# Kernel tuning notes

Hardware: AMD Instinct MI355X
Metric: run time of the kernel (lower is better)

The kernel has to match this reference:

```python
import jax, jax.numpy as jnp
import numpy as np

B, T, C = 2, 2048, 2048
N_HEAD, KV_HEADS = 16, 4
HEAD_DIM = C // N_HEAD  # 128
EPS = 1e-6


def setup_inputs() -> dict:
    key = jax.random.key(0)
    ks = jax.random.split(key, 3)
    x = jax.random.normal(ks[0], (B, T, C), dtype=jnp.float32)
    qkv_out = (N_HEAD + 2 * KV_HEADS) * HEAD_DIM  # 3072
    w_qkv = jax.random.normal(ks[1], (qkv_out, C), dtype=jnp.float32) * 0.02
    w_proj = jax.random.normal(ks[2], (C, C), dtype=jnp.float32) * 0.02
    q_norm_w = jnp.ones((HEAD_DIM,), dtype=jnp.float32)
    k_norm_w = jnp.ones((HEAD_DIM,), dtype=jnp.float32)
    # RoPE frequencies: theta = 10000^{-2i/d}, angles = pos * theta
    inv_freq = 1.0 / (10000.0 ** (np.arange(0, HEAD_DIM, 2, dtype=np.float32) / HEAD_DIM))
    angles = np.arange(T, dtype=np.float32)[:, None] * inv_freq[None, :]  # [T, 64]
    freqs_cos = jnp.asarray(np.cos(angles), dtype=jnp.float32)
    freqs_sin = jnp.asarray(np.sin(angles), dtype=jnp.float32)
    return {"x": x, "w_qkv": w_qkv, "w_proj": w_proj,
            "q_norm_w": q_norm_w, "k_norm_w": k_norm_w,
            "freqs_cos": freqs_cos, "freqs_sin": freqs_sin}


def _rope(t, cos, sin):
    # t: [B, H, T, D]; interpret last dim as D/2 complex pairs (a, b)
    a = t[..., 0::2]
    b = t[..., 1::2]
    oa = a * cos - b * sin
    ob = a * sin + b * cos
    return jnp.stack([oa, ob], axis=-1).reshape(t.shape)


def _rmsnorm(t, w, eps=EPS):
    rms = jnp.sqrt(jnp.mean(t * t, axis=-1, keepdims=True) + eps)
    return w * (t / rms)


def reference(x, w_qkv, w_proj, q_norm_w, k_norm_w, freqs_cos, freqs_sin):
    b, t, c = x.shape
    hd = HEAD_DIM
    qkv = x @ w_qkv.T  # [B, T, 3072]
    q_size = N_HEAD * hd
    kv_size = KV_HEADS * hd
    q = qkv[..., :q_size].reshape(b, t, N_HEAD, hd).transpose(0, 2, 1, 3)
    k = qkv[..., q_size:q_size + kv_size].reshape(b, t, KV_HEADS, hd).transpose(0, 2, 1, 3)
    v = qkv[..., q_size + kv_size:].reshape(b, t, KV_HEADS, hd).transpose(0, 2, 1, 3)
    # repeat_interleave KV heads to match query heads (GQA)
    rep = N_HEAD // KV_HEADS
    k = jnp.repeat(k, rep, axis=1)
    v = jnp.repeat(v, rep, axis=1)
    # RoPE (applied after repeat, matching the torch code order)
    cos = freqs_cos[:t][None, None, :, :]
    sin = freqs_sin[:t][None, None, :, :]
    q = _rope(q, cos, sin)
    k = _rope(k, cos, sin)
    # QK RMSNorm per head_dim
    q = _rmsnorm(q, q_norm_w)
    k = _rmsnorm(k, k_norm_w)
    # causal SDPA
    scores = jnp.einsum('bhqd,bhkd->bhqk', q, k) / jnp.sqrt(jnp.float32(hd))
    causal = jnp.tril(jnp.ones((t, t), dtype=bool))
    scores = jnp.where(causal[None, None], scores, jnp.finfo(scores.dtype).min)
    att = jax.nn.softmax(scores, axis=-1)
    y = jnp.einsum('bhqk,bhkd->bhqd', att, v)
    y = y.transpose(0, 2, 1, 3).reshape(b, t, c)
    return y @ w_proj.T
```

## Files before the change

### kernel.cpp

```cpp
#include <hip/hip_runtime.h>
#include <hip/hip_bf16.h>

#define B_    2
#define T_    2048
#define C_    2048
#define NH_   16
#define KVH_  4
#define HD_   128
#define QKV_  3072
#define M_    4096

typedef float  floatx4 __attribute__((ext_vector_type(4)));
typedef __bf16 bf16x8  __attribute__((ext_vector_type(8)));
typedef __bf16 bf16x4  __attribute__((ext_vector_type(4)));
typedef __bf16 bf16x2  __attribute__((ext_vector_type(2)));

typedef const __attribute__((address_space(1))) void* gas_t;
typedef __attribute__((address_space(3))) void*       las_t;
__device__ __forceinline__ void gl_lds16(const void* g, void* l) {
  __builtin_amdgcn_global_load_lds((gas_t)g, (las_t)l, 16, 0, 0);
}

__global__ __launch_bounds__(256) void cvt_bf16(const float* __restrict__ src,
                                                __bf16* __restrict__ dst, int n4) {
  int i = blockIdx.x * blockDim.x + threadIdx.x;
  if (i < n4) {
    float4 f = ((const float4*)src)[i];
    bf16x4 o = { (__bf16)f.x, (__bf16)f.y, (__bf16)f.z, (__bf16)f.w };
    ((bf16x4*)dst)[i] = o;
  }
}

__global__ __launch_bounds__(256) void gemm_bt(const __bf16* __restrict__ A,
                                               const __bf16* __restrict__ Bm,
                                               float* __restrict__ Cc,
                                               int N, int K) {
  __shared__ __align__(16) __bf16 As[128 * 32];
  __shared__ __align__(16) __bf16 Bs[128 * 32];
  const int tid  = threadIdx.x;
  const int wid  = tid >> 6, lane = tid & 63, quad = lane >> 4, r16 = lane & 15;
  const int bm   = blockIdx.y * 128, bn = blockIdx.x * 128;
  const int wm   = (wid >> 1) * 64, wn = (wid & 1) * 64;
  const int srow = wid * 16 + (lane >> 2);
  const int scol = (lane & 3) * 8;
  const __bf16* aptr = A  + (size_t)(bm + srow) * K + scol;
  const __bf16* bptr = Bm + (size_t)(bn + srow) * K + scol;
  __bf16* ldsA0 = &As[wid * 512];
  __bf16* ldsA1 = &As[2048 + wid * 512];
  __bf16* ldsB0 = &Bs[wid * 512];
  __bf16* ldsB1 = &Bs[2048 + wid * 512];
  const size_t rowskip = (size_t)64 * K;

  floatx4 acc[4][4];
  #pragma unroll
  for (int i = 0; i < 4; i++)
    #pragma unroll
    for (int j = 0; j < 4; j++) acc[i][j] = (floatx4){0.f, 0.f, 0.f, 0.f};

  for (int k0 = 0; k0 < K; k0 += 32) {
    gl_lds16(aptr + k0,           ldsA0);
    gl_lds16(aptr + rowskip + k0, ldsA1);
    gl_lds16(bptr + k0,           ldsB0);
    gl_lds16(bptr + rowskip + k0, ldsB1);
    __syncthreads();

    bf16x8 af[4], bfr[4];
    #pragma unroll
    for (int i = 0; i < 4; i++) af[i]  = *(const bf16x8*)&As[(wm + i * 16 + r16) * 32 + quad * 8];
    #pragma unroll
    for (int j = 0; j < 4; j++) bfr[j] = *(const bf16x8*)&Bs[(wn + j * 16 + r16) * 32 + quad * 8];

    #pragma unroll
    for (int i = 0; i < 4; i++)
      #pragma unroll
      for (int j = 0; j < 4; j++)
        acc[i][j] = __builtin_amdgcn_mfma_f32_16x16x32_bf16(af[i], bfr[j], acc[i][j], 0, 0, 0);
    __syncthreads();
  }

  #pragma unroll
  for (int i = 0; i < 4; i++) {
    #pragma unroll
    for (int reg = 0; reg < 4; reg++) {
      int row = bm + wm + i * 16 + quad * 4 + reg;
      float* crow = Cc + (size_t)row * N + bn + wn;
      #pragma unroll
      for (int j = 0; j < 4; j++) crow[j * 16 + r16] = acc[i][j][reg];
    }
  }
}

__global__ __launch_bounds__(256) void rope_norm(const float* __restrict__ qkv,
                                                 const float* __restrict__ qw,
                                                 const float* __restrict__ kw,
                                                 const float* __restrict__ fc,
                                                 const float* __restrict__ fs,
                                                 __bf16* __restrict__ qn,
                                                 __bf16* __restrict__ kn) {
  const int tid  = threadIdx.x;
  const int wid  = tid >> 6, lane = tid & 63;
  const int row  = blockIdx.x * 4 + wid;
  const int b    = row >> 11, t = row & (T_ - 1);
  const float cs = fc[t * 64 + lane], sn = fs[t * 64 + lane];
  const float* base = qkv + (size_t)row * QKV_;

  #pragma unroll 2
  for (int h = 0; h < NH_; h++) {
    float2 ab = *(const float2*)(base + h * HD_ + 2 * lane);
    float oa = ab.x * cs - ab.y * sn;
    float ob = ab.x * sn + ab.y * cs;
    float ss = oa * oa + ob * ob;
    #pragma unroll
    for (int off = 32; off; off >>= 1) ss += __shfl_xor(ss, off);
    float rinv = rsqrtf(ss * (1.0f / HD_) + 1e-6f);
    bf16x2 o = { (__bf16)(oa * rinv * qw[2 * lane]), (__bf16)(ob * rinv * qw[2 * lane + 1]) };
    *(bf16x2*)&qn[(size_t)((b * NH_ + h) * T_ + t) * HD_ + 2 * lane] = o;
  }
  #pragma unroll 2
  for (int h = 0; h < KVH_; h++) {
    float2 ab = *(const float2*)(base + C_ + h * HD_ + 2 * lane);
    float oa = ab.x * cs - ab.y * sn;
    float ob = ab.x * sn + ab.y * cs;
    float ss = oa * oa + ob * ob;
    #pragma unroll
    for (int off = 32; off; off >>= 1) ss += __shfl_xor(ss, off);
    float rinv = rsqrtf(ss * (1.0f / HD_) + 1e-6f);
    bf16x2 o = { (__bf16)(oa * rinv * kw[2 * lane]), (__bf16)(ob * rinv * kw[2 * lane + 1]) };
    *(bf16x2*)&kn[(size_t)((b * KVH_ + h) * T_ + t) * HD_ + 2 * lane] = o;
  }
}

__global__ __launch_bounds__(256) void vtrans(const float* __restrict__ qkv,
                                              __bf16* __restrict__ vT) {
  __shared__ __bf16 L[64 * 68];
  const int tid = threadIdx.x;
  const int t0 = blockIdx.x * 64;
  const int d0 = blockIdx.y * 64;
  const int z  = blockIdx.z;
  const int b  = z >> 2, hk = z & 3;
  const int srcc = C_ + KVH_ * HD_ + hk * HD_ + d0;
  const int rr = tid >> 4, c4 = (tid & 15) * 4;
  #pragma unroll
  for (int i = 0; i < 4; i++) {
    int t = rr + i * 16;
    float4 f = *(const float4*)&qkv[(size_t)(b * T_ + t0 + t) * QKV_ + srcc + c4];
    bf16x4 o = { (__bf16)f.x, (__bf16)f.y, (__bf16)f.z, (__bf16)f.w };
    *(bf16x4*)&L[t * 68 + c4] = o;
  }
  __syncthreads();
  const int dr = tid >> 3, tc8 = (tid & 7) * 8;
  #pragma unroll
  for (int i = 0; i < 2; i++) {
    int d = dr + i * 32;
    bf16x8 ov;
    #pragma unroll
    for (int j = 0; j < 8; j++) ov[j] = L[(tc8 + j) * 68 + d];
    *(bf16x8*)&vT[(size_t)(z * HD_ + d0 + d) * T_ + t0 + tc8] = ov;
  }
}

__device__ __forceinline__ void kv_prefetch(const __bf16* kbase, const __bf16* vbase,
                                            int kt0, int wid, int lane,
                                            bf16x8 kreg[4], bf16x8 vreg[4]) {
  const int r4 = lane >> 2, c8 = (lane & 3) * 8;
  const __bf16* kg = kbase + (size_t)(kt0 + wid * 16 + r4) * HD_ + c8;
  #pragma unroll
  for (int cb = 0; cb < 4; cb++) kreg[cb] = *(const bf16x8*)(kg + cb * 32);
  #pragma unroll
  for (int s = 0; s < 2; s++) {
    const __bf16* vg = vbase + (size_t)((wid * 2 + s) * 16 + r4) * T_ + kt0 + c8;
    #pragma unroll
    for (int cb = 0; cb < 2; cb++) vreg[s * 2 + cb] = *(const bf16x8*)(vg + cb * 32);
  }
}

__device__ __forceinline__ void kv_commit(__bf16* Ks, __bf16* Vs, int wid, int lane,
                                          const bf16x8 kreg[4], const bf16x8 vreg[4]) {
  #pragma unroll
  for (int cb = 0; cb < 4; cb++)
    *(bf16x8*)(Ks + wid * 2048 + cb * 512 + lane * 8) = kreg[cb];
  #pragma unroll
  for (int s = 0; s < 2; s++)
    #pragma unroll
    for (int cb = 0; cb < 2; cb++)
      *(bf16x8*)(Vs + (wid * 2 + s) * 1024 + cb * 512 + lane * 8) = vreg[s * 2 + cb];
}

__global__ __launch_bounds__(256) void flash(const __bf16* __restrict__ q,
                                             const __bf16* __restrict__ k,
                                             const __bf16* __restrict__ vT,
                                             __bf16* __restrict__ y) {
  __shared__ __align__(16) __bf16 Ks[64 * 128];
  __shared__ __align__(16) __bf16 Vs[128 * 64];
  __shared__ __align__(16) __bf16 Ps[4][16 * 72];
  const int tid = threadIdx.x;
  const int wid = tid >> 6, lane = tid & 63, quad = lane >> 4, r16 = lane & 15;
  const int h = blockIdx.y, b = blockIdx.z;
  const int hk = h >> 2;
  const __bf16* kbase = k  + (size_t)(b * KVH_ + hk) * T_ * HD_;
  const __bf16* vbase = vT + (size_t)(b * KVH_ + hk) * HD_ * T_;
  __bf16* Pw = Ps[wid];
  const float sc = 0.08838834764831845f;
  const float NEG = -__builtin_inff();
  bf16x8 ones;
  #pragma unroll
  for (int i = 0; i < 8; i++) ones[i] = (__bf16)1.0f;

  #pragma unroll 1
  for (int pass = 0; pass < 2; ++pass) {
    const int qt = pass ? blockIdx.x : (31 - blockIdx.x);
    const int nt = qt + 1;
    const int r0 = qt * 64 + wid * 16;

    const __bf16* qrow = q + ((size_t)(b * NH_ + h) * T_ + r0 + r16) * HD_;
    bf16x8 qf[4];
    #pragma unroll
    for (int kb = 0; kb < 4; kb++) qf[kb] = *(const bf16x8*)&qrow[kb * 32 + quad * 8];

    floatx4 o[8], ol = (floatx4){0.f, 0.f, 0.f, 0.f};
    #pragma unroll
    for (int j = 0; j < 8; j++) o[j] = (floatx4){0.f, 0.f, 0.f, 0.f};
    float m_r[4] = {NEG, NEG, NEG, NEG};

    bf16x8 kreg[4], vreg[4];
    kv_prefetch(kbase, vbase, 0, wid, lane, kreg, vreg);

    #pragma unroll 1
    for (int it = 0; it < nt; ++it) {
      __syncthreads();
      kv_commit(Ks, Vs, wid, lane, kreg, vreg);
      __syncthreads();
      if (it + 1 < nt) kv_prefetch(kbase, vbase, (it + 1) * 64, wid, lane, kreg, vreg);

      const int kt0 = it * 64;
      floatx4 s[4];
      #pragma unroll
      for (int cb = 0; cb < 4; cb++) s[cb] = (floatx4){0.f, 0.f, 0.f, 0.f};
      #pragma unroll
      for (int kb = 0; kb < 4; kb++)
        #pragma unroll
        for (int cb = 0; cb < 4; cb++) {
          bf16x8 kf = *(const bf16x8*)&Ks[(cb * 4 + kb) * 512 + r16 * 32 + quad * 8];
          s[cb] = __builtin_amdgcn_mfma_f32_16x16x32_bf16(qf[kb], kf, s[cb], 0, 0, 0);
        }

      const bool last = (it == nt - 1);
      float alpha[4];
      #pragma unroll
      for (int reg = 0; reg < 4; reg++) {
        const int rowq = r0 + quad * 4 + reg;
        float v0 = s[0][reg] * sc, v1 = s[1][reg] * sc, v2 = s[2][reg] * sc, v3 = s[3][reg] * sc;
        if (last) {
          if (kt0 +      r16 > rowq) v0 = NEG;
          if (kt0 + 16 + r16 > rowq) v1 = NEG;
          if (kt0 + 32 + r16 > rowq) v2 = NEG;
          if (kt0 + 48 + r16 > rowq) v3 = NEG;
        }
        float mx = fmaxf(fmaxf(v0, v1), fmaxf(v2, v3));
        #pragma unroll
        for (int off = 8; off; off >>= 1) mx = fmaxf(mx, __shfl_xor(mx, off));
        float mnew = fmaxf(m_r[reg], mx);
        alpha[reg] = __expf(m_r[reg] - mnew);
        m_r[reg] = mnew;
        Pw[(quad * 4 + reg) * 72 +      r16] = (__bf16)__expf(v0 - mnew);
        Pw[(quad * 4 + reg) * 72 + 16 + r16] = (__bf16)__expf(v1 - mnew);
        Pw[(quad * 4 + reg) * 72 + 32 + r16] = (__bf16)__expf(v2 - mnew);
        Pw[(quad * 4 + reg) * 72 + 48 + r16] = (__bf16)__expf(v3 - mnew);
      }
      #pragma unroll
      for (int reg = 0; reg < 4; reg++) {
        ol[reg] *= alpha[reg];
        #pragma unroll
        for (int j = 0; j < 8; j++) o[j][reg] *= alpha[reg];
      }
      __asm__ volatile("" ::: "memory");
      bf16x8 pf0 = *(const bf16x8*)&Pw[r16 * 72 + quad * 8];
      bf16x8 pf1 = *(const bf16x8*)&Pw[r16 * 72 + 32 + quad * 8];
      ol = __builtin_amdgcn_mfma_f32_16x16x32_bf16(pf0, ones, ol, 0, 0, 0);
      ol = __builtin_amdgcn_mfma_f32_16x16x32_bf16(pf1, ones, ol, 0, 0, 0);
      #pragma unroll
      for (int j = 0; j < 8; j++) {
        bf16x8 vf0 = *(const bf16x8*)&Vs[(j * 2 + 0) * 512 + r16 * 32 + quad * 8];
        bf16x8 vf1 = *(const bf16x8*)&Vs[(j * 2 + 1) * 512 + r16 * 32 + quad * 8];
        o[j] = __builtin_amdgcn_mfma_f32_16x16x32_bf16(pf0, vf0, o[j], 0, 0, 0);
        o[j] = __builtin_amdgcn_mfma_f32_16x16x32_bf16(pf1, vf1, o[j], 0, 0, 0);
      }
    }

    #pragma unroll
    for (int reg = 0; reg < 4; reg++) {
      int trow = r0 + quad * 4 + reg;
      float inv = 1.0f / ol[reg];
      __bf16* yr = y + ((size_t)(b * T_) + trow) * C_ + h * HD_;
      #pragma unroll
      for (int j = 0; j < 8; j++) yr[j * 16 + r16] = (__bf16)(o[j][reg] * inv);
    }
  }
}

extern "C" void kernel_launch(void* const* d_in, const int* in_sizes, int n_in,
                              void* d_out, int out_size, void* d_ws, size_t ws_size,
                              hipStream_t stream) {
  const float* x     = (const float*)d_in[0];
  const float* wqkv  = (const float*)d_in[1];
  const float* wproj = (const float*)d_in[2];
  const float* qw    = (const float*)d_in[3];
  const float* kw    = (const float*)d_in[4];
  const float* fc    = (const float*)d_in[5];
  const float* fs    = (const float*)d_in[6];
  float* out = (float*)d_out;

  char* w = (char*)d_ws;
  __bf16* xb     = (__bf16*)w; w += (size_t)M_ * C_ * 2;
  __bf16* wqkvb  = (__bf16*)w; w += (size_t)QKV_ * C_ * 2;
  __bf16* wprojb = (__bf16*)w; w += (size_t)C_ * C_ * 2;
  float*  qkv    = (float*)w;  w += (size_t)M_ * QKV_ * 4;
  __bf16* qn     = (__bf16*)w; w += (size_t)B_ * NH_ * T_ * HD_ * 2;
  __bf16* kn     = (__bf16*)w; w += (size_t)B_ * KVH_ * T_ * HD_ * 2;
  __bf16* vT     = (__bf16*)w; w += (size_t)B_ * KVH_ * T_ * HD_ * 2;
  __bf16* ybf    = (__bf16*)w; w += (size_t)M_ * C_ * 2;

  cvt_bf16<<<M_ * C_ / 4 / 256, 256, 0, stream>>>(x, xb, M_ * C_ / 4);
  cvt_bf16<<<QKV_ * C_ / 4 / 256, 256, 0, stream>>>(wqkv, wqkvb, QKV_ * C_ / 4);
  cvt_bf16<<<C_ * C_ / 4 / 256, 256, 0, stream>>>(wproj, wprojb, C_ * C_ / 4);

  gemm_bt<<<dim3(QKV_ / 128, M_ / 128), 256, 0, stream>>>(xb, wqkvb, qkv, QKV_, C_);
  rope_norm<<<M_ / 4, 256, 0, stream>>>(qkv, qw, kw, fc, fs, qn, kn);
  vtrans<<<dim3(T_ / 64, HD_ / 64, B_ * KVH_), 256, 0, stream>>>(qkv, vT);
  flash<<<dim3(16, NH_, B_), 256, 0, stream>>>(qn, kn, vT, ybf);
  gemm_bt<<<dim3(C_ / 128, M_ / 128), 256, 0, stream>>>(ybf, wprojb, out, C_, C_);
}
```

Measured before the change: 362.1 us.

## Merge conversions, store QKV in bf16, widen GEMM K-step, restructure flash blocks

The three fp32-to-bf16 conversions become a single launch. The QKV GEMM now writes bf16 instead of fp32, which halves the intermediate traffic read by rope_norm and vtrans. The GEMM loads two 32-wide K slices per barrier pair, halving the number of syncs. The flash kernel moves to 512-thread blocks covering 128 query rows over a flattened 256-block grid, and each warp skips KV tiles that lie entirely above its causal diagonal. Rounding QKV to bf16 before RoPE and the norm adds some precision loss.

Result: faster. 327.4 us (-9.6%).

```diff
diff --git a/kernel.cpp b/kernel.cpp
--- a/kernel.cpp
+++ b/kernel.cpp
@@ -21,22 +21,29 @@
   __builtin_amdgcn_global_load_lds((gas_t)g, (las_t)l, 16, 0, 0);
 }
 
-__global__ __launch_bounds__(256) void cvt_bf16(const float* __restrict__ src,
-                                                __bf16* __restrict__ dst, int n4) {
+__global__ __launch_bounds__(256) void cvt3(const float* __restrict__ s0, __bf16* __restrict__ d0, int n0,
+                                            const float* __restrict__ s1, __bf16* __restrict__ d1, int n1,
+                                            const float* __restrict__ s2, __bf16* __restrict__ d2, int n2) {
   int i = blockIdx.x * blockDim.x + threadIdx.x;
-  if (i < n4) {
-    float4 f = ((const float4*)src)[i];
-    bf16x4 o = { (__bf16)f.x, (__bf16)f.y, (__bf16)f.z, (__bf16)f.w };
-    ((bf16x4*)dst)[i] = o;
-  }
-}
-
+  const float* s; __bf16* d;
+  if (i < n0) { s = s0; d = d0; }
+  else {
+    i -= n0;
+    if (i < n1) { s = s1; d = d1; }
+    else { i -= n1; if (i >= n2) return; s = s2; d = d2; }
+  }
+  float4 f = ((const float4*)s)[i];
+  bf16x4 o = { (__bf16)f.x, (__bf16)f.y, (__bf16)f.z, (__bf16)f.w };
+  ((bf16x4*)d)[i] = o;
+}
+
+template <typename OutT>
 __global__ __launch_bounds__(256) void gemm_bt(const __bf16* __restrict__ A,
                                                const __bf16* __restrict__ Bm,
-                                               float* __restrict__ Cc,
+                                               OutT* __restrict__ Cc,
                                                int N, int K) {
-  __shared__ __align__(16) __bf16 As[128 * 32];
-  __shared__ __align__(16) __bf16 Bs[128 * 32];
+  __shared__ __align__(16) __bf16 As[2][128 * 32];
+  __shared__ __align__(16) __bf16 Bs[2][128 * 32];
   const int tid  = threadIdx.x;
   const int wid  = tid >> 6, lane = tid & 63, quad = lane >> 4, r16 = lane & 15;
   const int bm   = blockIdx.y * 128, bn = blockIdx.x * 128;
@@ -45,10 +52,6 @@
   const int scol = (lane & 3) * 8;
   const __bf16* aptr = A  + (size_t)(bm + srow) * K + scol;
   const __bf16* bptr = Bm + (size_t)(bn + srow) * K + scol;
-  __bf16* ldsA0 = &As[wid * 512];
-  __bf16* ldsA1 = &As[2048 + wid * 512];
-  __bf16* ldsB0 = &Bs[wid * 512];
-  __bf16* ldsB1 = &Bs[2048 + wid * 512];
   const size_t rowskip = (size_t)64 * K;
 
   floatx4 acc[4][4];
@@ -57,24 +60,29 @@
     #pragma unroll
     for (int j = 0; j < 4; j++) acc[i][j] = (floatx4){0.f, 0.f, 0.f, 0.f};
 
-  for (int k0 = 0; k0 < K; k0 += 32) {
-    gl_lds16(aptr + k0,           ldsA0);
-    gl_lds16(aptr + rowskip + k0, ldsA1);
-    gl_lds16(bptr + k0,           ldsB0);
-    gl_lds16(bptr + rowskip + k0, ldsB1);
+  for (int k0 = 0; k0 < K; k0 += 64) {
+    #pragma unroll
+    for (int hf = 0; hf < 2; hf++) {
+      gl_lds16(aptr + k0 + hf * 32,           &As[hf][wid * 512]);
+      gl_lds16(aptr + rowskip + k0 + hf * 32, &As[hf][2048 + wid * 512]);
+      gl_lds16(bptr + k0 + hf * 32,           &Bs[hf][wid * 512]);
+      gl_lds16(bptr + rowskip + k0 + hf * 32, &Bs[hf][2048 + wid * 512]);
+    }
     __syncthreads();
 
-    bf16x8 af[4], bfr[4];
-    #pragma unroll
-    for (int i = 0; i < 4; i++) af[i]  = *(const bf16x8*)&As[(wm + i * 16 + r16) * 32 + quad * 8];
-    #pragma unroll
-    for (int j = 0; j < 4; j++) bfr[j] = *(const bf16x8*)&Bs[(wn + j * 16 + r16) * 32 + quad * 8];
-
-    #pragma unroll
-    for (int i = 0; i < 4; i++)
-      #pragma unroll
-      for (int j = 0; j < 4; j++)
-        acc[i][j] = __builtin_amdgcn_mfma_f32_16x16x32_bf16(af[i], bfr[j], acc[i][j], 0, 0, 0);
+    #pragma unroll
+    for (int hf = 0; hf < 2; hf++) {
+      bf16x8 af[4], bfr[4];
+      #pragma unroll
+      for (int i = 0; i < 4; i++) af[i]  = *(const bf16x8*)&As[hf][(wm + i * 16 + r16) * 32 + quad * 8];
+      #pragma unroll
+      for (int j = 0; j < 4; j++) bfr[j] = *(const bf16x8*)&Bs[hf][(wn + j * 16 + r16) * 32 + quad * 8];
+      #pragma unroll
+      for (int i = 0; i < 4; i++)
+        #pragma unroll
+        for (int j = 0; j < 4; j++)
+          acc[i][j] = __builtin_amdgcn_mfma_f32_16x16x32_bf16(af[i], bfr[j], acc[i][j], 0, 0, 0);
+    }
     __syncthreads();
   }
 
@@ -83,14 +91,14 @@
     #pragma unroll
     for (int reg = 0; reg < 4; reg++) {
       int row = bm + wm + i * 16 + quad * 4 + reg;
-      float* crow = Cc + (size_t)row * N + bn + wn;
-      #pragma unroll
-      for (int j = 0; j < 4; j++) crow[j * 16 + r16] = acc[i][j][reg];
-    }
-  }
-}
-
-__global__ __launch_bounds__(256) void rope_norm(const float* __restrict__ qkv,
+      OutT* crow = Cc + (size_t)row * N + bn + wn;
+      #pragma unroll
+      for (int j = 0; j < 4; j++) crow[j * 16 + r16] = (OutT)acc[i][j][reg];
+    }
+  }
+}
+
+__global__ __launch_bounds__(256) void rope_norm(const __bf16* __restrict__ qkv,
                                                  const float* __restrict__ qw,
                                                  const float* __restrict__ kw,
                                                  const float* __restrict__ fc,
@@ -102,13 +110,14 @@
   const int row  = blockIdx.x * 4 + wid;
   const int b    = row >> 11, t = row & (T_ - 1);
   const float cs = fc[t * 64 + lane], sn = fs[t * 64 + lane];
-  const float* base = qkv + (size_t)row * QKV_;
+  const __bf16* base = qkv + (size_t)row * QKV_;
 
   #pragma unroll 2
   for (int h = 0; h < NH_; h++) {
-    float2 ab = *(const float2*)(base + h * HD_ + 2 * lane);
-    float oa = ab.x * cs - ab.y * sn;
-    float ob = ab.x * sn + ab.y * cs;
+    bf16x2 ab = *(const bf16x2*)(base + h * HD_ + 2 * lane);
+    float ax = (float)ab[0], ay = (float)ab[1];
+    float oa = ax * cs - ay * sn;
+    float ob = ax * sn + ay * cs;
     float ss = oa * oa + ob * ob;
     #pragma unroll
     for (int off = 32; off; off >>= 1) ss += __shfl_xor(ss, off);
@@ -118,9 +127,10 @@
   }
   #pragma unroll 2
   for (int h = 0; h < KVH_; h++) {
-    float2 ab = *(const float2*)(base + C_ + h * HD_ + 2 * lane);
-    float oa = ab.x * cs - ab.y * sn;
-    float ob = ab.x * sn + ab.y * cs;
+    bf16x2 ab = *(const bf16x2*)(base + C_ + h * HD_ + 2 * lane);
+    float ax = (float)ab[0], ay = (float)ab[1];
+    float oa = ax * cs - ay * sn;
+    float ob = ax * sn + ay * cs;
     float ss = oa * oa + ob * ob;
     #pragma unroll
     for (int off = 32; off; off >>= 1) ss += __shfl_xor(ss, off);
@@ -130,7 +140,7 @@
   }
 }
 
-__global__ __launch_bounds__(256) void vtrans(const float* __restrict__ qkv,
+__global__ __launch_bounds__(256) void vtrans(const __bf16* __restrict__ qkv,
                                               __bf16* __restrict__ vT) {
   __shared__ __bf16 L[64 * 68];
   const int tid = threadIdx.x;
@@ -143,9 +153,8 @@
   #pragma unroll
   for (int i = 0; i < 4; i++) {
     int t = rr + i * 16;
-    float4 f = *(const float4*)&qkv[(size_t)(b * T_ + t0 + t) * QKV_ + srcc + c4];
-    bf16x4 o = { (__bf16)f.x, (__bf16)f.y, (__bf16)f.z, (__bf16)f.w };
-    *(bf16x4*)&L[t * 68 + c4] = o;
+    bf16x4 f = *(const bf16x4*)&qkv[(size_t)(b * T_ + t0 + t) * QKV_ + srcc + c4];
+    *(bf16x4*)&L[t * 68 + c4] = f;
   }
   __syncthreads();
   const int dr = tid >> 3, tc8 = (tid & 7) * 8;
@@ -159,44 +168,40 @@
   }
 }
 
-__device__ __forceinline__ void kv_prefetch(const __bf16* kbase, const __bf16* vbase,
-                                            int kt0, int wid, int lane,
-                                            bf16x8 kreg[4], bf16x8 vreg[4]) {
+__device__ __forceinline__ void kv_prefetch8(const __bf16* kbase, const __bf16* vbase,
+                                             int kt0, int wid, int lane,
+                                             bf16x8 kreg[2], bf16x8 vreg[2]) {
   const int r4 = lane >> 2, c8 = (lane & 3) * 8;
-  const __bf16* kg = kbase + (size_t)(kt0 + wid * 16 + r4) * HD_ + c8;
-  #pragma unroll
-  for (int cb = 0; cb < 4; cb++) kreg[cb] = *(const bf16x8*)(kg + cb * 32);
-  #pragma unroll
-  for (int s = 0; s < 2; s++) {
-    const __bf16* vg = vbase + (size_t)((wid * 2 + s) * 16 + r4) * T_ + kt0 + c8;
-    #pragma unroll
-    for (int cb = 0; cb < 2; cb++) vreg[s * 2 + cb] = *(const bf16x8*)(vg + cb * 32);
-  }
-}
-
-__device__ __forceinline__ void kv_commit(__bf16* Ks, __bf16* Vs, int wid, int lane,
-                                          const bf16x8 kreg[4], const bf16x8 vreg[4]) {
-  #pragma unroll
-  for (int cb = 0; cb < 4; cb++)
-    *(bf16x8*)(Ks + wid * 2048 + cb * 512 + lane * 8) = kreg[cb];
-  #pragma unroll
-  for (int s = 0; s < 2; s++)
-    #pragma unroll
-    for (int cb = 0; cb < 2; cb++)
-      *(bf16x8*)(Vs + (wid * 2 + s) * 1024 + cb * 512 + lane * 8) = vreg[s * 2 + cb];
-}
-
-__global__ __launch_bounds__(256) void flash(const __bf16* __restrict__ q,
-                                             const __bf16* __restrict__ k,
-                                             const __bf16* __restrict__ vT,
-                                             __bf16* __restrict__ y) {
+  #pragma unroll
+  for (int i = 0; i < 2; i++) {
+    const int n = wid * 2 + i;
+    kreg[i] = *(const bf16x8*)&kbase[(size_t)(kt0 + (n >> 2) * 16 + r4) * HD_ + (n & 3) * 32 + c8];
+    vreg[i] = *(const bf16x8*)&vbase[(size_t)((n >> 1) * 16 + r4) * T_ + kt0 + (n & 1) * 32 + c8];
+  }
+}
+
+__device__ __forceinline__ void kv_commit8(__bf16* Ks, __bf16* Vs, int wid, int lane,
+                                           const bf16x8 kreg[2], const bf16x8 vreg[2]) {
+  #pragma unroll
+  for (int i = 0; i < 2; i++) {
+    *(bf16x8*)(Ks + (wid * 2 + i) * 512 + lane * 8) = kreg[i];
+    *(bf16x8*)(Vs + (wid * 2 + i) * 512 + lane * 8) = vreg[i];
+  }
+}
+
+__global__ __launch_bounds__(512, 2) void flash(const __bf16* __restrict__ q,
+                                                const __bf16* __restrict__ k,
+                                                const __bf16* __restrict__ vT,
+                                                __bf16* __restrict__ y) {
   __shared__ __align__(16) __bf16 Ks[64 * 128];
   __shared__ __align__(16) __bf16 Vs[128 * 64];
-  __shared__ __align__(16) __bf16 Ps[4][16 * 72];
+  __shared__ __align__(16) __bf16 Ps[8][16 * 72];
   const int tid = threadIdx.x;
   const int wid = tid >> 6, lane = tid & 63, quad = lane >> 4, r16 = lane & 15;
-  const int h = blockIdx.y, b = blockIdx.z;
-  const int hk = h >> 2;
+  const int x   = blockIdx.x;
+  const int pair = x >> 5, hl = x & 31;
+  const int b = hl >> 4, h = hl & 15, hk = h >> 2;
+
   const __bf16* kbase = k  + (size_t)(b * KVH_ + hk) * T_ * HD_;
   const __bf16* vbase = vT + (size_t)(b * KVH_ + hk) * HD_ * T_;
   __bf16* Pw = Ps[wid];
@@ -207,10 +212,10 @@
   for (int i = 0; i < 8; i++) ones[i] = (__bf16)1.0f;
 
   #pragma unroll 1
-  for (int pass = 0; pass < 2; ++pass) {
-    const int qt = pass ? blockIdx.x : (31 - blockIdx.x);
-    const int nt = qt + 1;
-    const int r0 = qt * 64 + wid * 16;
+  for (int seg = 0; seg < 2; ++seg) {
+    const int qt = seg ? pair : (15 - pair);
+    const int nt = 2 * (qt + 1);
+    const int r0 = qt * 128 + wid * 16;
 
     const __bf16* qrow = q + ((size_t)(b * NH_ + h) * T_ + r0 + r16) * HD_;
     bf16x8 qf[4];
@@ -222,68 +227,71 @@
     for (int j = 0; j < 8; j++) o[j] = (floatx4){0.f, 0.f, 0.f, 0.f};
     float m_r[4] = {NEG, NEG, NEG, NEG};
 
-    bf16x8 kreg[4], vreg[4];
-    kv_prefetch(kbase, vbase, 0, wid, lane, kreg, vreg);
+    bf16x8 kreg[2], vreg[2];
+    kv_prefetch8(kbase, vbase, 0, wid, lane, kreg, vreg);
 
     #pragma unroll 1
     for (int it = 0; it < nt; ++it) {
       __syncthreads();
-      kv_commit(Ks, Vs, wid, lane, kreg, vreg);
+      kv_commit8(Ks, Vs, wid, lane, kreg, vreg);
       __syncthreads();
-      if (it + 1 < nt) kv_prefetch(kbase, vbase, (it + 1) * 64, wid, lane, kreg, vreg);
+      if (it + 1 < nt) kv_prefetch8(kbase, vbase, (it + 1) * 64, wid, lane, kreg, vreg);
 
       const int kt0 = it * 64;
-      floatx4 s[4];
-      #pragma unroll
-      for (int cb = 0; cb < 4; cb++) s[cb] = (floatx4){0.f, 0.f, 0.f, 0.f};
-      #pragma unroll
-      for (int kb = 0; kb < 4; kb++)
-        #pragma unroll
-        for (int cb = 0; cb < 4; cb++) {
-          bf16x8 kf = *(const bf16x8*)&Ks[(cb * 4 + kb) * 512 + r16 * 32 + quad * 8];
-          s[cb] = __builtin_amdgcn_mfma_f32_16x16x32_bf16(qf[kb], kf, s[cb], 0, 0, 0);
+      if (kt0 <= r0 + 15) {
+        floatx4 s[4];
+        #pragma unroll
+        for (int cb = 0; cb < 4; cb++) s[cb] = (floatx4){0.f, 0.f, 0.f, 0.f};
+        #pragma unroll
+        for (int kb = 0; kb < 4; kb++)
+          #pragma unroll
+          for (int cb = 0; cb < 4; cb++) {
+            bf16x8 kf = *(const bf16x8*)&Ks[(cb * 4 + kb) * 512 + r16 * 32 + quad * 8];
+            s[cb] = __builtin_amdgcn_mfma_f32_16x16x32_bf16(qf[kb], kf, s[cb], 0, 0, 0);
+          }
+
+        const bool needmask = (kt0 + 63 > r0);
+        float alpha[4];
+        #pragma unroll
+        for (int reg = 0; reg < 4; reg++) {
+          const int rowq = r0 + quad * 4 + reg;
+          float v0 = s[0][reg] * sc, v1 = s[1][reg] * sc;
+          float v2 = s[2][reg] * sc, v3 = s[3][reg] * sc;
+          if (needmask) {
+            if (kt0 +      r16 > rowq) v0 = NEG;
+            if (kt0 + 16 + r16 > rowq) v1 = NEG;
+            if (kt0 + 32 + r16 > rowq) v2 = NEG;
+            if (kt0 + 48 + r16 > rowq) v3 = NEG;
+          }
+          float mx = fmaxf(fmaxf(v0, v1), fmaxf(v2, v3));
+          #pragma unroll
+          for (int off = 8; off; off >>= 1) mx = fmaxf(mx, __shfl_xor(mx, off));
+          float mnew = fmaxf(m_r[reg], mx);
+          alpha[reg] = __expf(m_r[reg] - mnew);
+          m_r[reg] = mnew;
+          Pw[(quad * 4 + reg) * 72 +      r16] = (__bf16)__expf(v0 - mnew);
+          Pw[(quad * 4 + reg) * 72 + 16 + r16] = (__bf16)__expf(v1 - mnew);
+          Pw[(quad * 4 + reg) * 72 + 32 + r16] = (__bf16)__expf(v2 - mnew);
+          Pw[(quad * 4 + reg) * 72 + 48 + r16] = (__bf16)__expf(v3 - mnew);
         }
-
-      const bool last = (it == nt - 1);
-      float alpha[4];
-      #pragma unroll
-      for (int reg = 0; reg < 4; reg++) {
-        const int rowq = r0 + quad * 4 + reg;
-        float v0 = s[0][reg] * sc, v1 = s[1][reg] * sc, v2 = s[2][reg] * sc, v3 = s[3][reg] * sc;
-        if (last) {
-          if (kt0 +      r16 > rowq) v0 = NEG;
-          if (kt0 + 16 + r16 > rowq) v1 = NEG;
-          if (kt0 + 32 + r16 > rowq) v2 = NEG;
-          if (kt0 + 48 + r16 > rowq) v3 = NEG;
+        #pragma unroll
+        for (int reg = 0; reg < 4; reg++) {
+          ol[reg] *= alpha[reg];
+          #pragma unroll
+          for (int j = 0; j < 8; j++) o[j][reg] *= alpha[reg];
         }
-        float mx = fmaxf(fmaxf(v0, v1), fmaxf(v2, v3));
-        #pragma unroll
-        for (int off = 8; off; off >>= 1) mx = fmaxf(mx, __shfl_xor(mx, off));
-        float mnew = fmaxf(m_r[reg], mx);
-        alpha[reg] = __expf(m_r[reg] - mnew);
-        m_r[reg] = mnew;
-        Pw[(quad * 4 + reg) * 72 +      r16] = (__bf16)__expf(v0 - mnew);
-        Pw[(quad * 4 + reg) * 72 + 16 + r16] = (__bf16)__expf(v1 - mnew);
-        Pw[(quad * 4 + reg) * 72 + 32 + r16] = (__bf16)__expf(v2 - mnew);
-        Pw[(quad * 4 + reg) * 72 + 48 + r16] = (__bf16)__expf(v3 - mnew);
-      }
-      #pragma unroll
-      for (int reg = 0; reg < 4; reg++) {
-        ol[reg] *= alpha[reg];
-        #pragma unroll
-        for (int j = 0; j < 8; j++) o[j][reg] *= alpha[reg];
-      }
-      __asm__ volatile("" ::: "memory");
-      bf16x8 pf0 = *(const bf16x8*)&Pw[r16 * 72 + quad * 8];
-      bf16x8 pf1 = *(const bf16x8*)&Pw[r16 * 72 + 32 + quad * 8];
-      ol = __builtin_amdgcn_mfma_f32_16x16x32_bf16(pf0, ones, ol, 0, 0, 0);
-      ol = __builtin_amdgcn_mfma_f32_16x16x32_bf16(pf1, ones, ol, 0, 0, 0);
-      #pragma unroll
-      for (int j = 0; j < 8; j++) {
-        bf16x8 vf0 = *(const bf16x8*)&Vs[(j * 2 + 0) * 512 + r16 * 32 + quad * 8];
-        bf16x8 vf1 = *(const bf16x8*)&Vs[(j * 2 + 1) * 512 + r16 * 32 + quad * 8];
-        o[j] = __builtin_amdgcn_mfma_f32_16x16x32_bf16(pf0, vf0, o[j], 0, 0, 0);
-        o[j] = __builtin_amdgcn_mfma_f32_16x16x32_bf16(pf1, vf1, o[j], 0, 0, 0);
+        __asm__ volatile("" ::: "memory");
+        bf16x8 pf0 = *(const bf16x8*)&Pw[r16 * 72 + quad * 8];
+        bf16x8 pf1 = *(const bf16x8*)&Pw[r16 * 72 + 32 + quad * 8];
+        ol = __builtin_amdgcn_mfma_f32_16x16x32_bf16(pf0, ones, ol, 0, 0, 0);
+        ol = __builtin_amdgcn_mfma_f32_16x16x32_bf16(pf1, ones, ol, 0, 0, 0);
+        #pragma unroll
+        for (int j = 0; j < 8; j++) {
+          bf16x8 vf0 = *(const bf16x8*)&Vs[(j * 2 + 0) * 512 + r16 * 32 + quad * 8];
+          bf16x8 vf1 = *(const bf16x8*)&Vs[(j * 2 + 1) * 512 + r16 * 32 + quad * 8];
+          o[j] = __builtin_amdgcn_mfma_f32_16x16x32_bf16(pf0, vf0, o[j], 0, 0, 0);
+          o[j] = __builtin_amdgcn_mfma_f32_16x16x32_bf16(pf1, vf1, o[j], 0, 0, 0);
+        }
       }
     }
 
@@ -314,19 +322,18 @@
   __bf16* xb     = (__bf16*)w; w += (size_t)M_ * C_ * 2;
   __bf16* wqkvb  = (__bf16*)w; w += (size_t)QKV_ * C_ * 2;
   __bf16* wprojb = (__bf16*)w; w += (size_t)C_ * C_ * 2;
-  float*  qkv    = (float*)w;  w += (size_t)M_ * QKV_ * 4;
+  __bf16* qkv    = (__bf16*)w; w += (size_t)M_ * QKV_ * 2;
   __bf16* qn     = (__bf16*)w; w += (size_t)B_ * NH_ * T_ * HD_ * 2;
   __bf16* kn     = (__bf16*)w; w += (size_t)B_ * KVH_ * T_ * HD_ * 2;
   __bf16* vT     = (__bf16*)w; w += (size_t)B_ * KVH_ * T_ * HD_ * 2;
   __bf16* ybf    = (__bf16*)w; w += (size_t)M_ * C_ * 2;
 
-  cvt_bf16<<<M_ * C_ / 4 / 256, 256, 0, stream>>>(x, xb, M_ * C_ / 4);
-  cvt_bf16<<<QKV_ * C_ / 4 / 256, 256, 0, stream>>>(wqkv, wqkvb, QKV_ * C_ / 4);
-  cvt_bf16<<<C_ * C_ / 4 / 256, 256, 0, stream>>>(wproj, wprojb, C_ * C_ / 4);
-
-  gemm_bt<<<dim3(QKV_ / 128, M_ / 128), 256, 0, stream>>>(xb, wqkvb, qkv, QKV_, C_);
+  const int n0 = M_ * C_ / 4, n1 = QKV_ * C_ / 4, n2 = C_ * C_ / 4;
+  cvt3<<<(n0 + n1 + n2 + 255) / 256, 256, 0, stream>>>(x, xb, n0, wqkv, wqkvb, n1, wproj, wprojb, n2);
+
+  gemm_bt<__bf16><<<dim3(QKV_ / 128, M_ / 128), 256, 0, stream>>>(xb, wqkvb, qkv, QKV_, C_);
   rope_norm<<<M_ / 4, 256, 0, stream>>>(qkv, qw, kw, fc, fs, qn, kn);
   vtrans<<<dim3(T_ / 64, HD_ / 64, B_ * KVH_), 256, 0, stream>>>(qkv, vT);
-  flash<<<dim3(16, NH_, B_), 256, 0, stream>>>(qn, kn, vT, ybf);
-  gemm_bt<<<dim3(C_ / 128, M_ / 128), 256, 0, stream>>>(ybf, wprojb, out, C_, C_);
-}
+  flash<<<dim3(256), 512, 0, stream>>>(qn, kn, vT, ybf);
+  gemm_bt<float><<<dim3(C_ / 128, M_ / 128), 256, 0, stream>>>(ybf, wprojb, out, C_, C_);
+}
```
